# Kernel tuning notes

Measured on AMD Instinct MI355X. Metric: run time of the kernel, lower is better.

The kernel has to match this reference:

```python
import jax, jax.numpy as jnp
import numpy as np
from jax import lax

B, T, C, H = 32, 2048, 256, 256
STRIDE = 2
TC = T // STRIDE  # 1024
NC1, NC2 = 100, 90
FC_IN = 2 * H * TC  # 524288
BN_EPS = 1e-5


def setup_inputs() -> dict:
    key = jax.random.key(0)
    ks = jax.random.split(key, 32)

    def n(k, shape, s=0.02):
        return jax.random.normal(k, shape, dtype=jnp.float32) * s

    inp = {
        "x": jax.random.normal(ks[0], (B, T), dtype=jnp.float32),
        # conv1d: in=1, out=C, k=3
        "conv_w": n(ks[1], (C, 1, 3), 0.3),
        "conv_b": jnp.zeros((C,), jnp.float32),
        # batchnorm (eval mode: running stats)
        "bn_g": jnp.ones((C,), jnp.float32),
        "bn_b": jnp.zeros((C,), jnp.float32),
        "bn_mean": jnp.zeros((C,), jnp.float32),
        "bn_var": jnp.ones((C,), jnp.float32),
        # LSTM layer 0 (input dim C), forward & reverse directions
        "w_ih_f0": n(ks[2], (4 * H, C)), "w_hh_f0": n(ks[3], (4 * H, H)), "b_f0": jnp.zeros((4 * H,), jnp.float32),
        "w_ih_r0": n(ks[4], (4 * H, C)), "w_hh_r0": n(ks[5], (4 * H, H)), "b_r0": jnp.zeros((4 * H,), jnp.float32),
        # LSTM layer 1 (input dim 2H)
        "w_ih_f1": n(ks[6], (4 * H, 2 * H)), "w_hh_f1": n(ks[7], (4 * H, H)), "b_f1": jnp.zeros((4 * H,), jnp.float32),
        "w_ih_r1": n(ks[8], (4 * H, 2 * H)), "w_hh_r1": n(ks[9], (4 * H, H)), "b_r1": jnp.zeros((4 * H,), jnp.float32),
        # dual FC heads over flattened [B, 2H*TC]
        "fc1_w": n(ks[10], (NC1, FC_IN), 0.005), "fc1_b": jnp.zeros((NC1,), jnp.float32),
        "fc2_w": n(ks[11], (NC2, FC_IN), 0.005), "fc2_b": jnp.zeros((NC2,), jnp.float32),
    }
    return inp


def _lstm_dir(xs, w_ih, w_hh, b, reverse):
    # xs: [B, T, D]. PyTorch gate order: i, f, g, o. bias = b_ih + b_hh fused.
    pre = jnp.einsum('btd,gd->btg', xs, w_ih) + b  # [B, T, 4H]
    if reverse:
        pre = pre[:, ::-1]
    bsz = xs.shape[0]
    h0 = jnp.zeros((bsz, H), xs.dtype)
    c0 = jnp.zeros((bsz, H), xs.dtype)

    def step(carry, gt):
        h, c = carry
        g = gt + h @ w_hh.T
        i, f, gg, o = jnp.split(g, 4, axis=-1)
        c = jax.nn.sigmoid(f) * c + jax.nn.sigmoid(i) * jnp.tanh(gg)
        h = jax.nn.sigmoid(o) * jnp.tanh(c)
        return (h, c), h

    _, hs = lax.scan(step, (h0, c0), jnp.swapaxes(pre, 0, 1))  # [T, B, H]
    hs = jnp.swapaxes(hs, 0, 1)
    if reverse:
        hs = hs[:, ::-1]
    return hs


def _bilstm(xs, w_ih_f, w_hh_f, b_f, w_ih_r, w_hh_r, b_r):
    hf = _lstm_dir(xs, w_ih_f, w_hh_f, b_f, False)
    hr = _lstm_dir(xs, w_ih_r, w_hh_r, b_r, True)
    return jnp.concatenate([hf, hr], axis=-1)  # [B, T, 2H]


def reference(x, conv_w, conv_b, bn_g, bn_b, bn_mean, bn_var,
              w_ih_f0, w_hh_f0, b_f0, w_ih_r0, w_hh_r0, b_r0,
              w_ih_f1, w_hh_f1, b_f1, w_ih_r1, w_hh_r1, b_r1,
              fc1_w, fc1_b, fc2_w, fc2_b):
    x3 = x[:, None, :]  # [B, 1, T]
    y = lax.conv_general_dilated(x3, conv_w, window_strides=(STRIDE,),
                                 padding=[(1, 1)],
                                 dimension_numbers=('NCH', 'OIH', 'NCH'))
    y = y + conv_b[None, :, None]  # [B, C, TC]
    # eval-mode BatchNorm1d + ReLU (Dropout1d is identity at eval)
    inv = bn_g * lax.rsqrt(bn_var + BN_EPS)
    y = jax.nn.relu(y * inv[None, :, None] + (bn_b - bn_mean * inv)[None, :, None])
    y = jnp.swapaxes(y, 1, 2)  # [B, TC, C]
    h = _bilstm(y, w_ih_f0, w_hh_f0, b_f0, w_ih_r0, w_hh_r0, b_r0)
    h = _bilstm(h, w_ih_f1, w_hh_f1, b_f1, w_ih_r1, w_hh_r1, b_r1)
    flat = h.reshape(h.shape[0], -1)  # [B, 2H*TC]
    out1 = flat @ fc1_w.T + fc1_b
    out2 = flat @ fc2_w.T + fc2_b
    return (out1, out2)
```

## Files before the change

kernel.cpp:

```cpp
#include <hip/hip_runtime.h>
#include <hip/hip_fp16.h>

typedef unsigned short u16;
typedef unsigned int   u32;

#define B_   32
#define T_   2048
#define C_   256
#define H_   256
#define TC_  1024
#define M_   (B_*TC_)

using bf16x8 = __attribute__((ext_vector_type(8))) short;
using f32x4  = __attribute__((ext_vector_type(4))) float;
typedef _Float16 f16x2 __attribute__((ext_vector_type(2)));

__device__ __forceinline__ u16 f2bf(float f) {
  u32 u = __float_as_uint(f);
  u32 r = u + 0x7fffu + ((u >> 16) & 1u);
  return (u16)(r >> 16);
}
__device__ __forceinline__ float sigmf(float x) { return 1.f / (1.f + __expf(-x)); }
__device__ __forceinline__ float tanhfast(float x) {
  float e = __expf(2.f * x);
  return 1.f - 2.f / (e + 1.f);
}
__device__ __forceinline__ float dot2(u32 w, u32 h, float acc) {
  return __builtin_amdgcn_fdot2(__builtin_bit_cast(f16x2, w),
                                __builtin_bit_cast(f16x2, h), acc, false);
}

__global__ void cast_bf16_kernel(const float* __restrict__ src, u16* __restrict__ dst, int n) {
  int i = blockIdx.x * 256 + threadIdx.x;
  if (i < n) dst[i] = f2bf(src[i]);
}
__global__ void cast_f16_kernel(const float* __restrict__ src, u16* __restrict__ dst, int n) {
  int i = blockIdx.x * 256 + threadIdx.x;
  if (i < n) dst[i] = __half_as_ushort(__float2half(src[i]));
}

__global__ __launch_bounds__(256)
void conv_bn_kernel(const float* __restrict__ x, const float* __restrict__ cw,
                    const float* __restrict__ cb, const float* __restrict__ bng,
                    const float* __restrict__ bnb, const float* __restrict__ bnm,
                    const float* __restrict__ bnv, u16* __restrict__ ybf) {
  int c = threadIdx.x;
  int bt = blockIdx.x;
  int t = bt & (TC_ - 1), b = bt >> 10;
  const float* xr = x + (size_t)b * T_;
  float xm1 = (t > 0) ? xr[2 * t - 1] : 0.f;
  float x0 = xr[2 * t], xp1 = xr[2 * t + 1];
  float w0 = cw[c * 3], w1 = cw[c * 3 + 1], w2 = cw[c * 3 + 2];
  float inv = bng[c] * rsqrtf(bnv[c] + 1e-5f);
  float beta = bnb[c] - bnm[c] * inv;
  float v = w0 * xm1 + w1 * x0 + w2 * xp1 + cb[c];
  v = v * inv + beta;
  v = fmaxf(v, 0.f);
  ybf[(size_t)bt * C_ + c] = f2bf(v);
}

#define PBK 32
#define APAD 8
__global__ __launch_bounds__(256)
void proj_gemm2_kernel(const u16* __restrict__ A,
                       const u16* __restrict__ Wf, const u16* __restrict__ Wr,
                       const float* __restrict__ bf, const float* __restrict__ br,
                       float* __restrict__ outf, float* __restrict__ outr,
                       int K) {
  const u16* W = blockIdx.z ? Wr : Wf;
  const float* bias = blockIdx.z ? br : bf;
  float* out = blockIdx.z ? outr : outf;
  __shared__ u16 As[128][PBK + APAD];
  __shared__ u16 Ws[128][PBK + APAD];
  const int tid = threadIdx.x;
  const int wave = tid >> 6, lane = tid & 63;
  const int l16 = lane & 15, quad = lane >> 4;
  const int m0 = blockIdx.x * 128, n0 = blockIdx.y * 128;
  const int wm = (wave >> 1) * 64, wn = (wave & 1) * 64;
  const int srow = tid >> 2, scol = (tid & 3) * 8;
  const u16* Ag0 = A + (size_t)(m0 + srow) * K + scol;
  const u16* Ag1 = Ag0 + (size_t)64 * K;
  const u16* Wg0 = W + (size_t)(n0 + srow) * K + scol;
  const u16* Wg1 = Wg0 + (size_t)64 * K;
  f32x4 acc[4][4] = {};
  for (int k0 = 0; k0 < K; k0 += PBK) {
    *(uint4*)&As[srow][scol]      = *(const uint4*)(Ag0 + k0);
    *(uint4*)&As[srow + 64][scol] = *(const uint4*)(Ag1 + k0);
    *(uint4*)&Ws[srow][scol]      = *(const uint4*)(Wg0 + k0);
    *(uint4*)&Ws[srow + 64][scol] = *(const uint4*)(Wg1 + k0);
    __syncthreads();
    bf16x8 af[4], wf[4];
#pragma unroll
    for (int i = 0; i < 4; ++i) {
      af[i] = *(const bf16x8*)&As[wm + 16 * i + l16][quad * 8];
      wf[i] = *(const bf16x8*)&Ws[wn + 16 * i + l16][quad * 8];
    }
#pragma unroll
    for (int i = 0; i < 4; ++i)
#pragma unroll
      for (int j = 0; j < 4; ++j)
        acc[i][j] = __builtin_amdgcn_mfma_f32_16x16x32_bf16(af[i], wf[j], acc[i][j], 0, 0, 0);
    __syncthreads();
  }
  float bv[4];
#pragma unroll
  for (int j = 0; j < 4; ++j) bv[j] = bias[n0 + wn + 16 * j + l16];
#pragma unroll
  for (int i = 0; i < 4; ++i) {
    int row = m0 + wm + 16 * i + quad * 4;
#pragma unroll
    for (int j = 0; j < 4; ++j) {
      int col = n0 + wn + 16 * j + l16;
#pragma unroll
      for (int r = 0; r < 4; ++r)
        out[(size_t)(row + r) * 1024 + col] = acc[i][j][r] + bv[j];
    }
  }
}

#define SCAN_LDS (131072 + 512 + 8192)
__global__ __launch_bounds__(1024, 1)
void scan3_kernel(const float* __restrict__ pre_f, const float* __restrict__ pre_r,
                  const u32* __restrict__ whh_f, const u32* __restrict__ whh_r,
                  void* __restrict__ outp, int out_bf16) {
  extern __shared__ char smem[];
  u32*   wlds  = (u32*)smem;
  u32*   hbuf  = (u32*)(smem + 131072);
  float* gpart = (float*)(smem + 131072 + 512);
  const int tid = threadIdx.x;
  const int p = tid & 511, kh = tid >> 9;
  const int chain = blockIdx.x;
  const int dir = chain & 1, b = chain >> 1;
  const float* pre = dir ? pre_r : pre_f;
  const u32* whh = dir ? whh_r : whh_f;

  u32 wreg0[48], wreg1[48];
  {
    const u32* w0p = whh + (size_t)p * 128 + kh * 64;
    const u32* w1p = w0p + (size_t)512 * 128;
#pragma unroll
    for (int c = 0; c < 12; ++c) {
      uint4 a = *(const uint4*)(w0p + c * 4);
      wreg0[c*4+0] = a.x; wreg0[c*4+1] = a.y; wreg0[c*4+2] = a.z; wreg0[c*4+3] = a.w;
      uint4 bq = *(const uint4*)(w1p + c * 4);
      wreg1[c*4+0] = bq.x; wreg1[c*4+1] = bq.y; wreg1[c*4+2] = bq.z; wreg1[c*4+3] = bq.w;
    }
#pragma unroll
    for (int c = 0; c < 4; ++c) {
      *(uint4*)(wlds + ((size_t)c * 1024 + tid) * 4)       = *(const uint4*)(w0p + (12 + c) * 4);
      *(uint4*)(wlds + ((size_t)(4 + c) * 1024 + tid) * 4) = *(const uint4*)(w1p + (12 + c) * 4);
    }
  }
  if (tid < 128) hbuf[tid] = 0u;
  float cst = 0.f;
  __syncthreads();

  const u32* hb = hbuf + kh * 64;
  float cur0 = 0.f, cur1 = 0.f;
  if (kh == 0) {
    const float* pr = pre + ((size_t)b * TC_ + (dir ? TC_ - 1 : 0)) * 1024;
    cur0 = pr[p]; cur1 = pr[p + 512];
  }
  for (int t = 0; t < TC_; ++t) {
    const int tt = dir ? (TC_ - 1 - t) : t;
    float nxt0 = 0.f, nxt1 = 0.f;
    if (kh == 0 && t + 1 < TC_) {
      const int tn = dir ? (TC_ - 2 - t) : (t + 1);
      const float* pr = pre + ((size_t)b * TC_ + tn) * 1024;
      nxt0 = pr[p]; nxt1 = pr[p + 512];
    }
    float acc0 = 0.f, acc1 = 0.f;
#pragma unroll
    for (int c = 0; c < 12; ++c) {
      uint4 h4 = *(const uint4*)(hb + c * 4);
      acc0 = dot2(wreg0[c*4+0], h4.x, acc0);
      acc0 = dot2(wreg0[c*4+1], h4.y, acc0);
      acc0 = dot2(wreg0[c*4+2], h4.z, acc0);
      acc0 = dot2(wreg0[c*4+3], h4.w, acc0);
      acc1 = dot2(wreg1[c*4+0], h4.x, acc1);
      acc1 = dot2(wreg1[c*4+1], h4.y, acc1);
      acc1 = dot2(wreg1[c*4+2], h4.z, acc1);
      acc1 = dot2(wreg1[c*4+3], h4.w, acc1);
    }
#pragma unroll
    for (int c = 0; c < 4; ++c) {
      uint4 h4 = *(const uint4*)(hb + (12 + c) * 4);
      uint4 w0 = *(const uint4*)(wlds + ((size_t)c * 1024 + tid) * 4);
      uint4 w1 = *(const uint4*)(wlds + ((size_t)(4 + c) * 1024 + tid) * 4);
      acc0 = dot2(w0.x, h4.x, acc0);
      acc0 = dot2(w0.y, h4.y, acc0);
      acc0 = dot2(w0.z, h4.z, acc0);
      acc0 = dot2(w0.w, h4.w, acc0);
      acc1 = dot2(w1.x, h4.x, acc1);
      acc1 = dot2(w1.y, h4.y, acc1);
      acc1 = dot2(w1.z, h4.z, acc1);
      acc1 = dot2(w1.w, h4.w, acc1);
    }
    if (kh == 0) { acc0 += cur0; acc1 += cur1; }
    gpart[kh * 1024 + p]       = acc0;
    gpart[kh * 1024 + p + 512] = acc1;
    __syncthreads();
    {
      float g = gpart[tid] + gpart[1024 + tid];
      float a = ((tid >> 8) == 2) ? tanhfast(g) : sigmf(g);
      gpart[tid] = a;
    }
    __syncthreads();
    if (tid < 256) {
      const int j = tid;
      float i_ = gpart[j], f_ = gpart[256 + j], g_ = gpart[512 + j], o_ = gpart[768 + j];
      cst = f_ * cst + i_ * g_;
      float h = o_ * tanhfast(cst);
      size_t oi = ((size_t)b * TC_ + tt) * 512 + (size_t)dir * 256 + j;
      if (out_bf16) ((u16*)outp)[oi] = f2bf(h);
      else          ((float*)outp)[oi] = h;
      u16 hu = __half_as_ushort(__float2half(h));
      u16 hn = (u16)__shfl_down((int)hu, 1);
      if ((j & 1) == 0) hbuf[j >> 1] = (u32)hu | ((u32)hn << 16);
    }
    cur0 = nxt0; cur1 = nxt1;
    __syncthreads();
  }
}

__global__ void fc_init_kernel(const float* __restrict__ fc1_b, const float* __restrict__ fc2_b,
                               float* __restrict__ out) {
  int i = blockIdx.x * 256 + threadIdx.x;
  if (i < 3200) out[i] = fc1_b[i % 100];
  else if (i < 6080) out[i] = fc2_b[(i - 3200) % 90];
}

#define FCK 1024
#define FCSUB 64
__global__ __launch_bounds__(256)
void fc_kernel(const float* __restrict__ flat, const float* __restrict__ w1,
               const float* __restrict__ w2, float* __restrict__ out) {
  __shared__ float fs[32][FCSUB + 1];
  __shared__ float ws[192][FCSUB + 1];
  int tid = threadIdx.x;
  int tn = tid & 31, tb = tid >> 5;
  size_t k0 = (size_t)blockIdx.x * FCK;
  float acc[4][6] = {};
  for (int kc = 0; kc < FCK; kc += FCSUB) {
    __syncthreads();
    for (int idx = tid; idx < 32 * FCSUB; idx += 256) {
      int bb = idx >> 6, j = idx & 63;
      fs[bb][j] = flat[(size_t)bb * 524288 + k0 + kc + j];
    }
    for (int idx = tid; idx < 192 * FCSUB; idx += 256) {
      int n = idx >> 6, j = idx & 63;
      float v = 0.f;
      if (n < 100)      v = w1[(size_t)n * 524288 + k0 + kc + j];
      else if (n < 190) v = w2[(size_t)(n - 100) * 524288 + k0 + kc + j];
      ws[n][j] = v;
    }
    __syncthreads();
    for (int j = 0; j < FCSUB; ++j) {
      float fv[4], wv[6];
#pragma unroll
      for (int m = 0; m < 4; ++m) fv[m] = fs[tb + 8 * m][j];
#pragma unroll
      for (int mm = 0; mm < 6; ++mm) wv[mm] = ws[tn + 32 * mm][j];
#pragma unroll
      for (int m = 0; m < 4; ++m)
#pragma unroll
        for (int mm = 0; mm < 6; ++mm) acc[m][mm] = fmaf(fv[m], wv[mm], acc[m][mm]);
    }
  }
#pragma unroll
  for (int m = 0; m < 4; ++m)
#pragma unroll
    for (int mm = 0; mm < 6; ++mm) {
      int n = tn + 32 * mm, bb = tb + 8 * m;
      if (n < 190) {
        int oi = (n < 100) ? (bb * 100 + n) : (3200 + bb * 90 + (n - 100));
        atomicAdd(out + oi, acc[m][mm]);
      }
    }
}

extern "C" void kernel_launch(void* const* d_in, const int* in_sizes, int n_in,
                              void* d_out, int out_size, void* d_ws, size_t ws_size,
                              hipStream_t stream) {
  const float* x       = (const float*)d_in[0];
  const float* conv_w  = (const float*)d_in[1];
  const float* conv_b  = (const float*)d_in[2];
  const float* bn_g    = (const float*)d_in[3];
  const float* bn_bb   = (const float*)d_in[4];
  const float* bn_m    = (const float*)d_in[5];
  const float* bn_v    = (const float*)d_in[6];
  const float* w_ih_f0 = (const float*)d_in[7];
  const float* w_hh_f0 = (const float*)d_in[8];
  const float* b_f0    = (const float*)d_in[9];
  const float* w_ih_r0 = (const float*)d_in[10];
  const float* w_hh_r0 = (const float*)d_in[11];
  const float* b_r0    = (const float*)d_in[12];
  const float* w_ih_f1 = (const float*)d_in[13];
  const float* w_hh_f1 = (const float*)d_in[14];
  const float* b_f1    = (const float*)d_in[15];
  const float* w_ih_r1 = (const float*)d_in[16];
  const float* w_hh_r1 = (const float*)d_in[17];
  const float* b_r1    = (const float*)d_in[18];
  const float* fc1_w   = (const float*)d_in[19];
  const float* fc1_b   = (const float*)d_in[20];
  const float* fc2_w   = (const float*)d_in[21];
  const float* fc2_b   = (const float*)d_in[22];
  float* out = (float*)d_out;

  char* base = (char*)d_ws;
  size_t off = 0;
  auto carve = [&](size_t bytes) -> char* {
    char* p = base + off;
    off += (bytes + 511) & ~(size_t)511;
    return p;
  };
  u16*   ybf   = (u16*)carve((size_t)M_ * 256 * 2);
  u16*   wb_f0 = (u16*)carve((size_t)262144 * 2);
  u16*   wb_r0 = (u16*)carve((size_t)262144 * 2);
  u16*   wb_f1 = (u16*)carve((size_t)524288 * 2);
  u16*   wb_r1 = (u16*)carve((size_t)524288 * 2);
  u16*   wh_f0 = (u16*)carve((size_t)262144 * 2);
  u16*   wh_r0 = (u16*)carve((size_t)262144 * 2);
  u16*   wh_f1 = (u16*)carve((size_t)262144 * 2);
  u16*   wh_r1 = (u16*)carve((size_t)262144 * 2);
  u16*   h0cat = (u16*)carve((size_t)M_ * 512 * 2);
  float* h1cat = (float*)carve((size_t)M_ * 512 * 4);
  float* pre_f = (float*)carve((size_t)M_ * 1024 * 4);
  float* pre_r = (float*)carve((size_t)M_ * 1024 * 4);
  if (off > ws_size) return;

  hipFuncSetAttribute((const void*)scan3_kernel,
                      hipFuncAttributeMaxDynamicSharedMemorySize, SCAN_LDS);

  cast_bf16_kernel<<<1024, 256, 0, stream>>>(w_ih_f0, wb_f0, 262144);
  cast_bf16_kernel<<<1024, 256, 0, stream>>>(w_ih_r0, wb_r0, 262144);
  cast_bf16_kernel<<<2048, 256, 0, stream>>>(w_ih_f1, wb_f1, 524288);
  cast_bf16_kernel<<<2048, 256, 0, stream>>>(w_ih_r1, wb_r1, 524288);
  cast_f16_kernel<<<1024, 256, 0, stream>>>(w_hh_f0, wh_f0, 262144);
  cast_f16_kernel<<<1024, 256, 0, stream>>>(w_hh_r0, wh_r0, 262144);
  cast_f16_kernel<<<1024, 256, 0, stream>>>(w_hh_f1, wh_f1, 262144);
  cast_f16_kernel<<<1024, 256, 0, stream>>>(w_hh_r1, wh_r1, 262144);

  conv_bn_kernel<<<M_, 256, 0, stream>>>(x, conv_w, conv_b, bn_g, bn_bb, bn_m, bn_v, ybf);

  proj_gemm2_kernel<<<dim3(256, 8, 2), 256, 0, stream>>>(
      ybf, wb_f0, wb_r0, b_f0, b_r0, pre_f, pre_r, 256);

  scan3_kernel<<<64, 1024, SCAN_LDS, stream>>>(
      pre_f, pre_r, (const u32*)wh_f0, (const u32*)wh_r0, (void*)h0cat, 1);

  proj_gemm2_kernel<<<dim3(256, 8, 2), 256, 0, stream>>>(
      h0cat, wb_f1, wb_r1, b_f1, b_r1, pre_f, pre_r, 512);

  scan3_kernel<<<64, 1024, SCAN_LDS, stream>>>(
      pre_f, pre_r, (const u32*)wh_f1, (const u32*)wh_r1, (void*)h1cat, 0);

  fc_init_kernel<<<24, 256, 0, stream>>>(fc1_b, fc2_b, out);
  fc_kernel<<<512, 256, 0, stream>>>(h1cat, fc1_w, fc2_w, out);
}
```

Before: 4.869 ms.

## Remap LSTM scan threads so gate combine uses wave shuffles, one barrier per step

Reassigns gate rows to lanes so that the two K-halves of each dot product and all four gates of a hidden unit sit in the same wavefront. Partial sums and gate activations are then combined with cross-lane shuffles instead of an LDS gpart buffer. The h buffer is double-buffered, so each timestep needs one __syncthreads instead of three. In exchange every thread now issues the pre-activation loads, and gate activations are computed redundantly across lanes. The leftover scoped block that computes an unused pointer has no effect.

```diff
diff --git a/kernel.cpp b/kernel.cpp
--- a/kernel.cpp
+++ b/kernel.cpp
@@ -118,17 +118,21 @@
   }
 }
 
-#define SCAN_LDS (131072 + 512 + 8192)
+#define SCAN_LDS (131072 + 1024)
 __global__ __launch_bounds__(1024, 1)
-void scan3_kernel(const float* __restrict__ pre_f, const float* __restrict__ pre_r,
+void scan4_kernel(const float* __restrict__ pre_f, const float* __restrict__ pre_r,
                   const u32* __restrict__ whh_f, const u32* __restrict__ whh_r,
                   void* __restrict__ outp, int out_bf16) {
   extern __shared__ char smem[];
-  u32*   wlds  = (u32*)smem;
-  u32*   hbuf  = (u32*)(smem + 131072);
-  float* gpart = (float*)(smem + 131072 + 512);
+  u32* wlds = (u32*)smem;
+  u32* hbuf = (u32*)(smem + 131072);
   const int tid = threadIdx.x;
-  const int p = tid & 511, kh = tid >> 9;
+  const int w = tid >> 6, l = tid & 63;
+  const int kh = l >> 5;
+  const int gsel = (l >> 4) & 1;
+  const int j = w * 16 + (l & 15);
+  const int row0 = gsel * 256 + j;
+  const int row1 = row0 + 512;
   const int chain = blockIdx.x;
   const int dir = chain & 1, b = chain >> 1;
   const float* pre = dir ? pre_r : pre_f;
@@ -136,8 +140,8 @@
 
   u32 wreg0[48], wreg1[48];
   {
-    const u32* w0p = whh + (size_t)p * 128 + kh * 64;
-    const u32* w1p = w0p + (size_t)512 * 128;
+    const u32* w0p = whh + (size_t)row0 * 128 + kh * 64;
+    const u32* w1p = whh + (size_t)row1 * 128 + kh * 64;
 #pragma unroll
     for (int c = 0; c < 12; ++c) {
       uint4 a = *(const uint4*)(w0p + c * 4);
@@ -151,23 +155,24 @@
       *(uint4*)(wlds + ((size_t)(4 + c) * 1024 + tid) * 4) = *(const uint4*)(w1p + (12 + c) * 4);
     }
   }
-  if (tid < 128) hbuf[tid] = 0u;
+  if (tid < 256) hbuf[tid] = 0u;
   float cst = 0.f;
+  {
+    const int t0 = dir ? TC_ - 1 : 0;
+    const float* pr = pre + ((size_t)b * TC_ + t0) * 1024;
+  }
+  const float* pr0 = pre + ((size_t)b * TC_ + (dir ? TC_ - 1 : 0)) * 1024;
+  float cur0 = pr0[row0], cur1 = pr0[row1];
   __syncthreads();
 
-  const u32* hb = hbuf + kh * 64;
-  float cur0 = 0.f, cur1 = 0.f;
-  if (kh == 0) {
-    const float* pr = pre + ((size_t)b * TC_ + (dir ? TC_ - 1 : 0)) * 1024;
-    cur0 = pr[p]; cur1 = pr[p + 512];
-  }
   for (int t = 0; t < TC_; ++t) {
     const int tt = dir ? (TC_ - 1 - t) : t;
+    const u32* hb = hbuf + (t & 1) * 128 + kh * 64;
     float nxt0 = 0.f, nxt1 = 0.f;
-    if (kh == 0 && t + 1 < TC_) {
+    if (t + 1 < TC_) {
       const int tn = dir ? (TC_ - 2 - t) : (t + 1);
       const float* pr = pre + ((size_t)b * TC_ + tn) * 1024;
-      nxt0 = pr[p]; nxt1 = pr[p + 512];
+      nxt0 = pr[row0]; nxt1 = pr[row1];
     }
     float acc0 = 0.f, acc1 = 0.f;
 #pragma unroll
@@ -196,27 +201,29 @@
       acc1 = dot2(w1.z, h4.z, acc1);
       acc1 = dot2(w1.w, h4.w, acc1);
     }
-    if (kh == 0) { acc0 += cur0; acc1 += cur1; }
-    gpart[kh * 1024 + p]       = acc0;
-    gpart[kh * 1024 + p + 512] = acc1;
-    __syncthreads();
-    {
-      float g = gpart[tid] + gpart[1024 + tid];
-      float a = ((tid >> 8) == 2) ? tanhfast(g) : sigmf(g);
-      gpart[tid] = a;
-    }
-    __syncthreads();
-    if (tid < 256) {
-      const int j = tid;
-      float i_ = gpart[j], f_ = gpart[256 + j], g_ = gpart[512 + j], o_ = gpart[768 + j];
-      cst = f_ * cst + i_ * g_;
-      float h = o_ * tanhfast(cst);
+    acc0 += __shfl_xor(acc0, 32);
+    acc1 += __shfl_xor(acc1, 32);
+    acc0 += cur0;
+    acc1 += cur1;
+    float a0 = sigmf(acc0);
+    float ax = gsel ? -acc1 : 2.f * acc1;
+    float e  = __expf(ax);
+    float r  = 1.f / (e + 1.f);
+    float a1 = gsel ? r : 1.f - 2.f * r;
+    float b0 = __shfl_xor(a0, 16);
+    float b1 = __shfl_xor(a1, 16);
+    float i_ = gsel ? b0 : a0;
+    float f_ = gsel ? a0 : b0;
+    float g_ = gsel ? b1 : a1;
+    float o_ = gsel ? a1 : b1;
+    cst = f_ * cst + i_ * g_;
+    float h = o_ * tanhfast(cst);
+    if (l < 16) {
       size_t oi = ((size_t)b * TC_ + tt) * 512 + (size_t)dir * 256 + j;
       if (out_bf16) ((u16*)outp)[oi] = f2bf(h);
       else          ((float*)outp)[oi] = h;
-      u16 hu = __half_as_ushort(__float2half(h));
-      u16 hn = (u16)__shfl_down((int)hu, 1);
-      if ((j & 1) == 0) hbuf[j >> 1] = (u32)hu | ((u32)hn << 16);
+      u16* hw = (u16*)(hbuf + ((t + 1) & 1) * 128);
+      hw[j] = __half_as_ushort(__float2half(h));
     }
     cur0 = nxt0; cur1 = nxt1;
     __syncthreads();
@@ -329,7 +336,7 @@
   float* pre_r = (float*)carve((size_t)M_ * 1024 * 4);
   if (off > ws_size) return;
 
-  hipFuncSetAttribute((const void*)scan3_kernel,
+  hipFuncSetAttribute((const void*)scan4_kernel,
                       hipFuncAttributeMaxDynamicSharedMemorySize, SCAN_LDS);
 
   cast_bf16_kernel<<<1024, 256, 0, stream>>>(w_ih_f0, wb_f0, 262144);
@@ -346,13 +353,13 @@
   proj_gemm2_kernel<<<dim3(256, 8, 2), 256, 0, stream>>>(
       ybf, wb_f0, wb_r0, b_f0, b_r0, pre_f, pre_r, 256);
 
-  scan3_kernel<<<64, 1024, SCAN_LDS, stream>>>(
+  scan4_kernel<<<64, 1024, SCAN_LDS, stream>>>(
       pre_f, pre_r, (const u32*)wh_f0, (const u32*)wh_r0, (void*)h0cat, 1);
 
   proj_gemm2_kernel<<<dim3(256, 8, 2), 256, 0, stream>>>(
       h0cat, wb_f1, wb_r1, b_f1, b_r1, pre_f, pre_r, 512);
 
-  scan3_kernel<<<64, 1024, SCAN_LDS, stream>>>(
+  scan4_kernel<<<64, 1024, SCAN_LDS, stream>>>(
       pre_f, pre_r, (const u32*)wh_f1, (const u32*)wh_r1, (void*)h1cat, 0);
 
   fc_init_kernel<<<24, 256, 0, stream>>>(fc1_b, fc2_b, out);
```

Measured after the change: 5.030 ms. 1.03x slower.

## Restructure LSTM scan to 256 threads with DPP quad reductions and one barrier

Applied to the files above, without the earlier changes.

Rewrites the recurrent scan kernel so each block of 256 threads assigns four lanes per hidden unit. Each lane covers a quarter of K for all four gates, and partial sums are combined with DPP quad reductions instead of an LDS gate-partial exchange. This removes two of the three barriers per timestep, uses a double-buffered h vector, and computes gate activations and the cell update in every thread. In exchange, each thread holds 96 uint4 of weights in registers, which risks heavy VGPR pressure or spills, and the pre-activation prefetch of the next step is dropped.

```diff
diff --git a/kernel.cpp b/kernel.cpp
--- a/kernel.cpp
+++ b/kernel.cpp
@@ -28,6 +28,12 @@
 __device__ __forceinline__ float dot2(u32 w, u32 h, float acc) {
   return __builtin_amdgcn_fdot2(__builtin_bit_cast(f16x2, w),
                                 __builtin_bit_cast(f16x2, h), acc, false);
+}
+__device__ __forceinline__ float qsum4(float x) {
+  int a = __builtin_amdgcn_update_dpp(0, __float_as_int(x), 0xB1, 0xF, 0xF, true);
+  x += __int_as_float(a);
+  int b = __builtin_amdgcn_update_dpp(0, __float_as_int(x), 0x4E, 0xF, 0xF, true);
+  return x + __int_as_float(b);
 }
 
 __global__ void cast_bf16_kernel(const float* __restrict__ src, u16* __restrict__ dst, int n) {
@@ -118,107 +124,88 @@
   }
 }
 
-#define SCAN_LDS (131072 + 512 + 8192)
-__global__ __launch_bounds__(1024, 1)
-void scan3_kernel(const float* __restrict__ pre_f, const float* __restrict__ pre_r,
+#define SCAN5_LDS (131072 + 1024)
+__global__ __launch_bounds__(256, 1)
+void scan5_kernel(const float* __restrict__ pre_f, const float* __restrict__ pre_r,
                   const u32* __restrict__ whh_f, const u32* __restrict__ whh_r,
                   void* __restrict__ outp, int out_bf16) {
   extern __shared__ char smem[];
-  u32*   wlds  = (u32*)smem;
-  u32*   hbuf  = (u32*)(smem + 131072);
-  float* gpart = (float*)(smem + 131072 + 512);
+  uint4* wlds = (uint4*)smem;
+  u16*   hbuf = (u16*)(smem + 131072);
   const int tid = threadIdx.x;
-  const int p = tid & 511, kh = tid >> 9;
+  const int p = tid >> 2, kq = tid & 3;
   const int chain = blockIdx.x;
   const int dir = chain & 1, b = chain >> 1;
   const float* pre = dir ? pre_r : pre_f;
   const u32* whh = dir ? whh_r : whh_f;
 
-  u32 wreg0[48], wreg1[48];
-  {
-    const u32* w0p = whh + (size_t)p * 128 + kh * 64;
-    const u32* w1p = w0p + (size_t)512 * 128;
-#pragma unroll
-    for (int c = 0; c < 12; ++c) {
-      uint4 a = *(const uint4*)(w0p + c * 4);
-      wreg0[c*4+0] = a.x; wreg0[c*4+1] = a.y; wreg0[c*4+2] = a.z; wreg0[c*4+3] = a.w;
-      uint4 bq = *(const uint4*)(w1p + c * 4);
-      wreg1[c*4+0] = bq.x; wreg1[c*4+1] = bq.y; wreg1[c*4+2] = bq.z; wreg1[c*4+3] = bq.w;
-    }
-#pragma unroll
-    for (int c = 0; c < 4; ++c) {
-      *(uint4*)(wlds + ((size_t)c * 1024 + tid) * 4)       = *(const uint4*)(w0p + (12 + c) * 4);
-      *(uint4*)(wlds + ((size_t)(4 + c) * 1024 + tid) * 4) = *(const uint4*)(w1p + (12 + c) * 4);
-    }
-  }
-  if (tid < 128) hbuf[tid] = 0u;
+  uint4 wr[12][8];
+#pragma unroll
+  for (int a = 0; a < 3; ++a)
+#pragma unroll
+    for (int g = 0; g < 4; ++g) {
+      const u32* wp = whh + (size_t)(p + 64 * a + 256 * g) * 128 + kq * 32;
+#pragma unroll
+      for (int i = 0; i < 8; ++i) wr[a * 4 + g][i] = *(const uint4*)(wp + i * 4);
+    }
+#pragma unroll
+  for (int g = 0; g < 4; ++g) {
+    const u32* wp = whh + (size_t)(p + 192 + 256 * g) * 128 + kq * 32;
+#pragma unroll
+    for (int i = 0; i < 8; ++i) wlds[(g * 8 + i) * 256 + tid] = *(const uint4*)(wp + i * 4);
+  }
+  hbuf[tid] = 0u;
   float cst = 0.f;
   __syncthreads();
 
-  const u32* hb = hbuf + kh * 64;
-  float cur0 = 0.f, cur1 = 0.f;
-  if (kh == 0) {
-    const float* pr = pre + ((size_t)b * TC_ + (dir ? TC_ - 1 : 0)) * 1024;
-    cur0 = pr[p]; cur1 = pr[p + 512];
-  }
+  const int j = p + 64 * kq;
   for (int t = 0; t < TC_; ++t) {
     const int tt = dir ? (TC_ - 1 - t) : t;
-    float nxt0 = 0.f, nxt1 = 0.f;
-    if (kh == 0 && t + 1 < TC_) {
-      const int tn = dir ? (TC_ - 2 - t) : (t + 1);
-      const float* pr = pre + ((size_t)b * TC_ + tn) * 1024;
-      nxt0 = pr[p]; nxt1 = pr[p + 512];
-    }
-    float acc0 = 0.f, acc1 = 0.f;
-#pragma unroll
-    for (int c = 0; c < 12; ++c) {
-      uint4 h4 = *(const uint4*)(hb + c * 4);
-      acc0 = dot2(wreg0[c*4+0], h4.x, acc0);
-      acc0 = dot2(wreg0[c*4+1], h4.y, acc0);
-      acc0 = dot2(wreg0[c*4+2], h4.z, acc0);
-      acc0 = dot2(wreg0[c*4+3], h4.w, acc0);
-      acc1 = dot2(wreg1[c*4+0], h4.x, acc1);
-      acc1 = dot2(wreg1[c*4+1], h4.y, acc1);
-      acc1 = dot2(wreg1[c*4+2], h4.z, acc1);
-      acc1 = dot2(wreg1[c*4+3], h4.w, acc1);
-    }
-#pragma unroll
-    for (int c = 0; c < 4; ++c) {
-      uint4 h4 = *(const uint4*)(hb + (12 + c) * 4);
-      uint4 w0 = *(const uint4*)(wlds + ((size_t)c * 1024 + tid) * 4);
-      uint4 w1 = *(const uint4*)(wlds + ((size_t)(4 + c) * 1024 + tid) * 4);
-      acc0 = dot2(w0.x, h4.x, acc0);
-      acc0 = dot2(w0.y, h4.y, acc0);
-      acc0 = dot2(w0.z, h4.z, acc0);
-      acc0 = dot2(w0.w, h4.w, acc0);
-      acc1 = dot2(w1.x, h4.x, acc1);
-      acc1 = dot2(w1.y, h4.y, acc1);
-      acc1 = dot2(w1.z, h4.z, acc1);
-      acc1 = dot2(w1.w, h4.w, acc1);
-    }
-    if (kh == 0) { acc0 += cur0; acc1 += cur1; }
-    gpart[kh * 1024 + p]       = acc0;
-    gpart[kh * 1024 + p + 512] = acc1;
-    __syncthreads();
-    {
-      float g = gpart[tid] + gpart[1024 + tid];
-      float a = ((tid >> 8) == 2) ? tanhfast(g) : sigmf(g);
-      gpart[tid] = a;
-    }
-    __syncthreads();
-    if (tid < 256) {
-      const int j = tid;
-      float i_ = gpart[j], f_ = gpart[256 + j], g_ = gpart[512 + j], o_ = gpart[768 + j];
-      cst = f_ * cst + i_ * g_;
-      float h = o_ * tanhfast(cst);
-      size_t oi = ((size_t)b * TC_ + tt) * 512 + (size_t)dir * 256 + j;
-      if (out_bf16) ((u16*)outp)[oi] = f2bf(h);
-      else          ((float*)outp)[oi] = h;
-      u16 hu = __half_as_ushort(__float2half(h));
-      u16 hn = (u16)__shfl_down((int)hu, 1);
-      if ((j & 1) == 0) hbuf[j >> 1] = (u32)hu | ((u32)hn << 16);
-    }
-    cur0 = nxt0; cur1 = nxt1;
+    const float* pr = pre + ((size_t)b * TC_ + tt) * 1024 + j;
+    float pv0 = pr[0], pv1 = pr[256], pv2 = pr[512], pv3 = pr[768];
+
+    const uint4* hq = (const uint4*)(hbuf + (t & 1) * 256) + kq * 8;
+    float acc[12] = {};
+    float accL[4] = {};
+#pragma unroll
+    for (int i = 0; i < 8; ++i) {
+      uint4 h4 = hq[i];
+#pragma unroll
+      for (int m = 0; m < 12; ++m) {
+        acc[m] = dot2(wr[m][i].x, h4.x, acc[m]);
+        acc[m] = dot2(wr[m][i].y, h4.y, acc[m]);
+        acc[m] = dot2(wr[m][i].z, h4.z, acc[m]);
+        acc[m] = dot2(wr[m][i].w, h4.w, acc[m]);
+      }
+#pragma unroll
+      for (int g = 0; g < 4; ++g) {
+        uint4 wv = wlds[(g * 8 + i) * 256 + tid];
+        accL[g] = dot2(wv.x, h4.x, accL[g]);
+        accL[g] = dot2(wv.y, h4.y, accL[g]);
+        accL[g] = dot2(wv.z, h4.z, accL[g]);
+        accL[g] = dot2(wv.w, h4.w, accL[g]);
+      }
+    }
+#pragma unroll
+    for (int m = 0; m < 12; ++m) acc[m] = qsum4(acc[m]);
+#pragma unroll
+    for (int g = 0; g < 4; ++g) accL[g] = qsum4(accL[g]);
+    float pg[4];
+#pragma unroll
+    for (int g = 0; g < 4; ++g) {
+      float v = (kq == 0) ? acc[g] : (kq == 1) ? acc[4 + g] : (kq == 2) ? acc[8 + g] : accL[g];
+      pg[g] = v;
+    }
+    float i_ = sigmf(pg[0] + pv0);
+    float f_ = sigmf(pg[1] + pv1);
+    float g_ = tanhfast(pg[2] + pv2);
+    float o_ = sigmf(pg[3] + pv3);
+    cst = f_ * cst + i_ * g_;
+    float h = o_ * tanhfast(cst);
+    hbuf[((t + 1) & 1) * 256 + j] = __half_as_ushort(__float2half(h));
+    size_t oi = ((size_t)b * TC_ + tt) * 512 + (size_t)dir * 256 + j;
+    if (out_bf16) ((u16*)outp)[oi] = f2bf(h);
+    else          ((float*)outp)[oi] = h;
     __syncthreads();
   }
 }
@@ -329,8 +316,8 @@
   float* pre_r = (float*)carve((size_t)M_ * 1024 * 4);
   if (off > ws_size) return;
 
-  hipFuncSetAttribute((const void*)scan3_kernel,
-                      hipFuncAttributeMaxDynamicSharedMemorySize, SCAN_LDS);
+  hipFuncSetAttribute((const void*)scan5_kernel,
+                      hipFuncAttributeMaxDynamicSharedMemorySize, SCAN5_LDS);
 
   cast_bf16_kernel<<<1024, 256, 0, stream>>>(w_ih_f0, wb_f0, 262144);
   cast_bf16_kernel<<<1024, 256, 0, stream>>>(w_ih_r0, wb_r0, 262144);
@@ -346,13 +333,13 @@
   proj_gemm2_kernel<<<dim3(256, 8, 2), 256, 0, stream>>>(
       ybf, wb_f0, wb_r0, b_f0, b_r0, pre_f, pre_r, 256);
 
-  scan3_kernel<<<64, 1024, SCAN_LDS, stream>>>(
+  scan5_kernel<<<64, 256, SCAN5_LDS, stream>>>(
       pre_f, pre_r, (const u32*)wh_f0, (const u32*)wh_r0, (void*)h0cat, 1);
 
   proj_gemm2_kernel<<<dim3(256, 8, 2), 256, 0, stream>>>(
       h0cat, wb_f1, wb_r1, b_f1, b_r1, pre_f, pre_r, 512);
 
-  scan3_kernel<<<64, 1024, SCAN_LDS, stream>>>(
+  scan5_kernel<<<64, 256, SCAN5_LDS, stream>>>(
       pre_f, pre_r, (const u32*)wh_f1, (const u32*)wh_r1, (void*)h1cat, 0);
 
   fc_init_kernel<<<24, 256, 0, stream>>>(fc1_b, fc2_b, out);
```

Result: slower. 6.671 ms (+37.0%).
